# Kernel tuning notes

Measured on AMD Instinct MI355X. Metric: run time of the kernel, lower is better.

## Reference

```python
import jax, jax.numpy as jnp
import numpy as np

N, E, B, D, DEPTH = 20000, 160000, 16, 128, 5
L = 4 * DEPTH  # 20 EGNN layer calls: (ground, ground_to_sub, sub, sub_to_ground) x depth


def _ln(x, g, b):
    mu = jnp.mean(x, -1, keepdims=True)
    var = jnp.mean((x - mu) ** 2, -1, keepdims=True)
    return (x - mu) * jax.lax.rsqrt(var + 1e-5) * g + b


def setup_inputs() -> dict:
    key = jax.random.key(0)
    ks = jax.random.split(key, 24)

    def w(k, shape, fan_in):
        return jax.random.normal(k, shape, jnp.float32) / np.float32(np.sqrt(fan_in))

    return {
        "x": jax.random.normal(ks[0], (N, 1), jnp.float32),
        "pos": jax.random.normal(ks[1], (N, 3), jnp.float32),
        "edge_index": jax.random.randint(ks[2], (2, E), 0, N),
        "node_subnode_index": jax.random.randint(ks[3], (2, E), 0, N),
        "subgraph_edge_index": jax.random.randint(ks[4], (2, E), 0, N),
        "subnode_node_index": jax.random.randint(ks[5], (2, E), 0, N),
        "batch_ids": jnp.sort(jax.random.randint(ks[6], (N,), 0, B)),
        "emb_W": w(ks[7], (1, D), 1), "emb_b": jnp.zeros((D,), jnp.float32),
        # message MLP: Linear(2D+1,D) -> LN -> SiLU -> Linear(D,D) -> LN -> SiLU, stacked over L layers
        "Wm1": w(ks[8], (L, 2 * D + 1, D), 2 * D + 1), "bm1": jnp.zeros((L, D), jnp.float32),
        "gm1": jnp.ones((L, D), jnp.float32), "sm1": jnp.zeros((L, D), jnp.float32),
        "Wm2": w(ks[9], (L, D, D), D), "bm2": jnp.zeros((L, D), jnp.float32),
        "gm2": jnp.ones((L, D), jnp.float32), "sm2": jnp.zeros((L, D), jnp.float32),
        # update MLP: Linear(2D,D) -> LN -> SiLU -> Linear(D,D) -> LN -> SiLU
        "Wu1": w(ks[10], (L, 2 * D, D), 2 * D), "bu1": jnp.zeros((L, D), jnp.float32),
        "gu1": jnp.ones((L, D), jnp.float32), "su1": jnp.zeros((L, D), jnp.float32),
        "Wu2": w(ks[11], (L, D, D), D), "bu2": jnp.zeros((L, D), jnp.float32),
        "gu2": jnp.ones((L, D), jnp.float32), "su2": jnp.zeros((L, D), jnp.float32),
        # prediction head: Linear(D,D) -> ReLU -> Linear(D,1)
        "pred_W1": w(ks[12], (D, D), D), "pred_b1": jnp.zeros((D,), jnp.float32),
        "pred_W2": w(ks[13], (D, 1), D), "pred_b2": jnp.zeros((1,), jnp.float32),
    }


def _egnn(h, pos, ei, i, Wm1, bm1, gm1, sm1, Wm2, bm2, gm2, sm2,
          Wu1, bu1, gu1, su1, Wu2, bu2, gu2, su2):
    src, dst = ei[0], ei[1]          # PyG: messages flow source -> target
    rel = pos[dst] - pos[src]
    dist = jnp.sqrt(jnp.sum(rel * rel, -1, keepdims=True))  # [E,1]
    m = jnp.concatenate([h[dst], h[src], dist], -1)          # [E, 2D+1] = [h_i, h_j, d]
    m = jax.nn.silu(_ln(m @ Wm1[i] + bm1[i], gm1[i], sm1[i]))
    m = jax.nn.silu(_ln(m @ Wm2[i] + bm2[i], gm2[i], sm2[i]))
    agg = jax.ops.segment_sum(m, dst, num_segments=h.shape[0])
    u = jnp.concatenate([h, agg], -1)                        # [N, 2D]
    u = jax.nn.silu(_ln(u @ Wu1[i] + bu1[i], gu1[i], su1[i]))
    u = jax.nn.silu(_ln(u @ Wu2[i] + bu2[i], gu2[i], su2[i]))
    return u


def reference(x, pos, edge_index, node_subnode_index, subgraph_edge_index,
              subnode_node_index, batch_ids, emb_W, emb_b,
              Wm1, bm1, gm1, sm1, Wm2, bm2, gm2, sm2,
              Wu1, bu1, gu1, su1, Wu2, bu2, gu2, su2,
              pred_W1, pred_b1, pred_W2, pred_b2):
    p = (Wm1, bm1, gm1, sm1, Wm2, bm2, gm2, sm2,
         Wu1, bu1, gu1, su1, Wu2, bu2, gu2, su2)
    h = x @ emb_W + emb_b
    edge_sets = (edge_index, node_subnode_index, subgraph_edge_index, subnode_node_index)
    for layer_idx in range(DEPTH):
        h0 = h
        for r, ei in enumerate(edge_sets):
            h = _egnn(h, pos, ei, layer_idx * 4 + r, *p)
        h = h + h0  # residual across the 4 message-passing steps
    out = jax.ops.segment_sum(h, batch_ids, num_segments=B)  # global_add_pool
    return jax.nn.relu(out @ pred_W1 + pred_b1) @ pred_W2 + pred_b2
```

## Files before the change

### kernel.cpp

```cpp
#include <hip/hip_runtime.h>

#define NN 20000
#define NE 160000
#define NL 20

typedef float f32x4 __attribute__((ext_vector_type(4)));
typedef float f32x2 __attribute__((ext_vector_type(2)));
typedef __bf16 bf16x8 __attribute__((ext_vector_type(8)));
typedef __bf16 bf16x4 __attribute__((ext_vector_type(4)));

__device__ __forceinline__ float silu_f(float v) {
  return v * __builtin_amdgcn_rcpf(1.f + __expf(-v));
}

__global__ void pack_weights(const float* __restrict__ W, __bf16* __restrict__ out,
                             const int K, const int lstride, const int total) {
  const int idx = blockIdx.x * 256 + threadIdx.x;
  if (idx >= total) return;
  const int lane = idx & 63;
  const int nt = (idx >> 6) & 7;
  const int ktn = K >> 5;
  const int kt = (idx >> 9) % ktn;
  const int layer = (idx >> 9) / ktn;
  const int col = nt * 16 + (lane & 15);
  const int kb = kt * 32 + (lane >> 4) * 8;
  const float* src = W + (size_t)layer * lstride;
  __bf16* o = out + (size_t)idx * 8;
#pragma unroll
  for (int j = 0; j < 8; ++j) o[j] = (__bf16)src[(kb + j) * 128 + col];
}

__global__ void pack_w1pq(const float* __restrict__ Wm1, __bf16* __restrict__ out) {
  const int idx = blockIdx.x * 256 + threadIdx.x;
  const int lane = idx & 63;
  const int nt = (idx >> 6) & 15;
  const int kt = (idx >> 10) & 3;
  const int layer = idx >> 12;
  const int c = nt * 16 + (lane & 15);
  const int kb = kt * 32 + (lane >> 4) * 8;
  const float* src = Wm1 + (size_t)layer * 257 * 128;
  __bf16* o = out + (size_t)idx * 8;
#pragma unroll
  for (int j = 0; j < 8; ++j) {
    const int k = kb + j;
    o[j] = (__bf16)((c < 128) ? src[k * 128 + c] : src[(128 + k) * 128 + (c - 128)]);
  }
}

__global__ void embed_kernel(const float* __restrict__ x, const float* __restrict__ embW,
                             const float* __restrict__ embB,
                             float* __restrict__ h, float* __restrict__ h0,
                             __bf16* __restrict__ hbf) {
  const int idx = blockIdx.x * 256 + threadIdx.x;
  const int n = idx >> 7, d = idx & 127;
  const float v = x[n] * embW[d] + embB[d];
  h[idx] = v;
  h0[idx] = v;
  hbf[idx] = (__bf16)v;
}

__global__ void hist_kernel(const int* __restrict__ ei, int* __restrict__ deg) {
  const int e = blockIdx.x * 256 + threadIdx.x;
  atomicAdd(&deg[ei[NE + e]], 1);
}

__global__ void scan_kernel(const int* __restrict__ deg, int* __restrict__ rowstart) {
  __shared__ int part[1024];
  const int r = blockIdx.x, t = threadIdx.x;
  const int* d = deg + (size_t)r * NN;
  int* rs = rowstart + (size_t)r * NN;
  int loc[20];
  int cnt = 0;
#pragma unroll
  for (int j = 0; j < 20; ++j) {
    const int i = t * 20 + j;
    const int v = (i < NN) ? d[i] : 0;
    loc[j] = cnt; cnt += v;
  }
  part[t] = cnt;
  __syncthreads();
  for (int off = 1; off < 1024; off <<= 1) {
    const int v = (t >= off) ? part[t - off] : 0;
    __syncthreads();
    part[t] += v;
    __syncthreads();
  }
  const int excl = (t == 0) ? 0 : part[t - 1];
#pragma unroll
  for (int j = 0; j < 20; ++j) {
    const int i = t * 20 + j;
    if (i < NN) rs[i] = excl + loc[j];
  }
}

__global__ void fill_kernel(const int* __restrict__ ei, const int* __restrict__ rowstart,
                            int* __restrict__ cursor, int* __restrict__ eord) {
  const int e = blockIdx.x * 256 + threadIdx.x;
  const int d = ei[NE + e];
  const int p = atomicAdd(&cursor[d], 1);
  eord[rowstart[d] + p] = e;
}

__global__ __launch_bounds__(256) void pq_kernel(
    const __bf16* __restrict__ hbf, const __bf16* __restrict__ pqw,
    __bf16* __restrict__ pq) {
  __shared__ __bf16 T1s[4][2048];
  const int t = threadIdx.x, w = t >> 6, l = t & 63;
  const int lr = l & 15, lg = l >> 4;
  const int wid = blockIdx.x * 4 + w;
  const int n0 = (wid >> 1) * 16;
  const int half = wid & 1;
  char* T1 = (char*)T1s[w];

  const int node = n0 + lr;
  bf16x8 bq[4];
#pragma unroll
  for (int kt = 0; kt < 4; ++kt)
    bq[kt] = *(const bf16x8*)(hbf + (size_t)node * 128 + kt * 32 + lg * 8);

  f32x4 acc[8];
#pragma unroll
  for (int nt = 0; nt < 8; ++nt) acc[nt] = (f32x4)0.f;
#pragma unroll
  for (int kt = 0; kt < 4; ++kt) {
#pragma unroll
    for (int nt = 0; nt < 8; ++nt) {
      const bf16x8 a = *(const bf16x8*)(pqw + ((size_t)((kt * 16 + half * 8 + nt) * 64 + l)) * 8);
      acc[nt] = __builtin_amdgcn_mfma_f32_16x16x32_bf16(a, bq[kt], acc[nt], 0, 0, 0);
    }
  }
#pragma unroll
  for (int nt = 0; nt < 8; ++nt) {
    bf16x4 v;
#pragma unroll
    for (int r = 0; r < 4; ++r) v[r] = (__bf16)acc[nt][r];
    *(bf16x4*)(T1 + ((lr * 256 + nt * 32 + lg * 8) ^ ((lr & 7) << 4))) = v;
  }
  __builtin_amdgcn_s_waitcnt(0);
#pragma unroll
  for (int j = 0; j < 4; ++j) {
    const int row = j * 4 + lg;
    const uint4 v = *(const uint4*)(T1 + ((row * 256 + lr * 16) ^ ((row & 7) << 4)));
    *(uint4*)(pq + (size_t)(n0 + row) * 256 + half * 128 + lr * 8) = v;
  }
}

__global__ __launch_bounds__(1024, 4) void edge_msg_kernel(
    const __bf16* __restrict__ pq, const float* __restrict__ pos,
    const int* __restrict__ ei, __bf16* __restrict__ msg,
    const __bf16* __restrict__ w2p, const float* __restrict__ w1last,
    const float* __restrict__ bm1, const float* __restrict__ gm1, const float* __restrict__ sm1,
    const float* __restrict__ bm2, const float* __restrict__ gm2, const float* __restrict__ sm2) {
  extern __shared__ char lds[];
  {
    const int t = threadIdx.x;
    uint4* d = (uint4*)lds;
    const uint4* s2 = (const uint4*)w2p;
    d[t] = s2[t];
    d[t + 1024] = s2[t + 1024];
  }
  __syncthreads();

  const int t = threadIdx.x, w = t >> 6, l = t & 63;
  const int lr = l & 15, lg = l >> 4;
  char* W2L = lds;
  char* T1  = lds + 32768 + w * 4096;

  const int e0 = blockIdx.x * 256 + w * 16;
  const int es = ei[e0 + lr], ed = ei[NE + e0 + lr];
  const float dx = pos[ed * 3 + 0] - pos[es * 3 + 0];
  const float dy = pos[ed * 3 + 1] - pos[es * 3 + 1];
  const float dz = pos[ed * 3 + 2] - pos[es * 3 + 2];
  const float dist = sqrtf(dx * dx + dy * dy + dz * dz);

  float v[4][8];
#pragma unroll
  for (int kt = 0; kt < 4; ++kt) {
    const int d0 = kt * 32 + lg * 8;
    const bf16x8 pA = *(const bf16x8*)(pq + (size_t)ed * 256 + d0);
    const bf16x8 qA = *(const bf16x8*)(pq + (size_t)es * 256 + 128 + d0);
    const f32x4 wl0 = *(const f32x4*)(w1last + d0), wl1 = *(const f32x4*)(w1last + d0 + 4);
    const f32x4 bb0 = *(const f32x4*)(bm1 + d0),    bb1 = *(const f32x4*)(bm1 + d0 + 4);
#pragma unroll
    for (int j = 0; j < 4; ++j) {
      v[kt][j]     = (float)pA[j]     + (float)qA[j]     + dist * wl0[j] + bb0[j];
      v[kt][j + 4] = (float)pA[j + 4] + (float)qA[j + 4] + dist * wl1[j] + bb1[j];
    }
  }
  float s = 0.f, q = 0.f;
#pragma unroll
  for (int kt = 0; kt < 4; ++kt)
#pragma unroll
    for (int j = 0; j < 8; ++j) { const float x = v[kt][j]; s += x; q += x * x; }
  s += __shfl_xor(s, 16); q += __shfl_xor(q, 16);
  s += __shfl_xor(s, 32); q += __shfl_xor(q, 32);
  const float mu1 = s * 0.0078125f;
  const float rstd1 = rsqrtf(q * 0.0078125f - mu1 * mu1 + 1e-5f);
  bf16x8 bfrag[4];
#pragma unroll
  for (int kt = 0; kt < 4; ++kt) {
    const int d0 = kt * 32 + lg * 8;
    const f32x4 g0 = *(const f32x4*)(gm1 + d0), g1 = *(const f32x4*)(gm1 + d0 + 4);
    const f32x4 s0 = *(const f32x4*)(sm1 + d0), s1 = *(const f32x4*)(sm1 + d0 + 4);
    bf16x8 bf;
#pragma unroll
    for (int j = 0; j < 4; ++j) {
      bf[j]     = (__bf16)silu_f((v[kt][j]     - mu1) * rstd1 * g0[j] + s0[j]);
      bf[j + 4] = (__bf16)silu_f((v[kt][j + 4] - mu1) * rstd1 * g1[j] + s1[j]);
    }
    bfrag[kt] = bf;
  }
  f32x4 acc2[8];
#pragma unroll
  for (int nt = 0; nt < 8; ++nt)
    acc2[nt] = *(const f32x4*)(bm2 + nt * 16 + lg * 4);
#pragma unroll
  for (int kt = 0; kt < 4; ++kt) {
#pragma unroll
    for (int nt = 0; nt < 8; ++nt) {
      const bf16x8 a = *(const bf16x8*)(W2L + ((kt * 8 + nt) * 64 + l) * 16);
      acc2[nt] = __builtin_amdgcn_mfma_f32_16x16x32_bf16(a, bfrag[kt], acc2[nt], 0, 0, 0);
    }
  }
  float s2 = 0.f, q2 = 0.f;
#pragma unroll
  for (int nt = 0; nt < 8; ++nt)
#pragma unroll
    for (int r = 0; r < 4; ++r) { const float x = acc2[nt][r]; s2 += x; q2 += x * x; }
  s2 += __shfl_xor(s2, 16); q2 += __shfl_xor(q2, 16);
  s2 += __shfl_xor(s2, 32); q2 += __shfl_xor(q2, 32);
  const float mu2 = s2 * 0.0078125f;
  const float rstd2 = rsqrtf(q2 * 0.0078125f - mu2 * mu2 + 1e-5f);
#pragma unroll
  for (int nt = 0; nt < 8; ++nt) {
    const f32x4 g2 = *(const f32x4*)(gm2 + nt * 16 + lg * 4);
    const f32x4 b2 = *(const f32x4*)(sm2 + nt * 16 + lg * 4);
    bf16x4 pk;
#pragma unroll
    for (int r = 0; r < 4; ++r)
      pk[r] = (__bf16)silu_f((acc2[nt][r] - mu2) * rstd2 * g2[r] + b2[r]);
    *(bf16x4*)(T1 + ((lr * 256 + nt * 32 + lg * 8) ^ ((lr & 7) << 4))) = pk;
  }
  __builtin_amdgcn_s_waitcnt(0);
  char* mbase = (char*)(msg + (size_t)e0 * 128);
#pragma unroll
  for (int j = 0; j < 4; ++j) {
    const int row = j * 4 + lg;
    const uint4 val = *(const uint4*)(T1 + ((row * 256 + lr * 16) ^ ((row & 7) << 4)));
    *(uint4*)(mbase + j * 1024 + l * 16) = val;
  }
}

__global__ void gather_kernel(const __bf16* __restrict__ msg,
                              const int* __restrict__ rowstart, const int* __restrict__ deg,
                              const int* __restrict__ eord, float* __restrict__ agg) {
  const int t = blockIdx.x * 256 + threadIdx.x;
  const int n = t >> 6, pd = t & 63;
  const int s = rowstart[n], dg = deg[n];
  float a0 = 0.f, a1 = 0.f;
  int i = 0;
  for (; i + 2 <= dg; i += 2) {
    const unsigned v0 = *(const unsigned*)(msg + (size_t)eord[s + i] * 128 + pd * 2);
    const unsigned v1 = *(const unsigned*)(msg + (size_t)eord[s + i + 1] * 128 + pd * 2);
    a0 += __uint_as_float(v0 << 16) + __uint_as_float(v1 << 16);
    a1 += __uint_as_float(v0 & 0xFFFF0000u) + __uint_as_float(v1 & 0xFFFF0000u);
  }
  if (i < dg) {
    const unsigned v0 = *(const unsigned*)(msg + (size_t)eord[s + i] * 128 + pd * 2);
    a0 += __uint_as_float(v0 << 16);
    a1 += __uint_as_float(v0 & 0xFFFF0000u);
  }
  f32x2 o; o[0] = a0; o[1] = a1;
  *(f32x2*)(agg + (size_t)n * 128 + pd * 2) = o;
}

__global__ __launch_bounds__(256) void update_kernel(
    float* __restrict__ h, const float* __restrict__ aggv, __bf16* __restrict__ hbf,
    float* __restrict__ h0, const int mode,
    const __bf16* __restrict__ w1p, const __bf16* __restrict__ w2p,
    const float* __restrict__ bu1, const float* __restrict__ gu1, const float* __restrict__ su1,
    const float* __restrict__ bu2, const float* __restrict__ gu2, const float* __restrict__ su2) {
  __shared__ __bf16 T1s[4][16 * 128];
  const int t = threadIdx.x, w = t >> 6, l = t & 63;
  const int lr = l & 15, lg = l >> 4;
  char* T1 = (char*)T1s[w];
  const int n0 = blockIdx.x * 64 + w * 16;
  const int n = n0 + lr;
  const int valid = (n < NN);
  const int nc = valid ? n : 0;

  bf16x8 ah[4], af[4];
#pragma unroll
  for (int kt = 0; kt < 4; ++kt) {
    ah[kt] = *(const bf16x8*)(hbf + (size_t)nc * 128 + kt * 32 + lg * 8);
    const f32x4* pA = (const f32x4*)(aggv + (size_t)nc * 128 + kt * 32 + lg * 8);
    const f32x4 u0 = pA[0], u1 = pA[1];
#pragma unroll
    for (int j = 0; j < 4; ++j) {
      af[kt][j] = (__bf16)u0[j];
      af[kt][j + 4] = (__bf16)u1[j];
    }
  }
  f32x4 acc[8];
#pragma unroll
  for (int nt = 0; nt < 8; ++nt) {
    const float bb = bu1[nt * 16 + lr];
#pragma unroll
    for (int r = 0; r < 4; ++r) acc[nt][r] = bb;
  }
#pragma unroll
  for (int kt = 0; kt < 8; ++kt) {
    const bf16x8 a = (kt < 4) ? ah[kt] : af[kt - 4];
#pragma unroll
    for (int nt = 0; nt < 8; ++nt) {
      const bf16x8 b = *(const bf16x8*)(w1p + ((size_t)((kt * 8 + nt) * 64 + l)) * 8);
      acc[nt] = __builtin_amdgcn_mfma_f32_16x16x32_bf16(a, b, acc[nt], 0, 0, 0);
    }
  }
  {
    float g1c[8], s1c[8];
#pragma unroll
    for (int nt = 0; nt < 8; ++nt) { g1c[nt] = gu1[nt * 16 + lr]; s1c[nt] = su1[nt * 16 + lr]; }
#pragma unroll
    for (int r = 0; r < 4; ++r) {
      float s = 0.f, q = 0.f;
#pragma unroll
      for (int nt = 0; nt < 8; ++nt) { const float v = acc[nt][r]; s += v; q += v * v; }
#pragma unroll
      for (int m = 1; m < 16; m <<= 1) { s += __shfl_xor(s, m); q += __shfl_xor(q, m); }
      const float mu = s * 0.0078125f;
      const float rstd = rsqrtf(q * 0.0078125f - mu * mu + 1e-5f);
      const int row = lg * 4 + r;
#pragma unroll
      for (int nt = 0; nt < 8; ++nt) {
        float v = (acc[nt][r] - mu) * rstd * g1c[nt] + s1c[nt];
        v = silu_f(v);
        const int col = nt * 16 + lr;
        *(__bf16*)(T1 + ((row * 256 + col * 2) ^ ((row & 7) << 4))) = (__bf16)v;
      }
    }
  }
  __syncthreads();
  f32x4 acc2[8];
#pragma unroll
  for (int nt = 0; nt < 8; ++nt) {
    const float bb = bu2[nt * 16 + lr];
#pragma unroll
    for (int r = 0; r < 4; ++r) acc2[nt][r] = bb;
  }
#pragma unroll
  for (int kt = 0; kt < 4; ++kt) {
    const bf16x8 a = *(const bf16x8*)(T1 + ((lr * 256 + kt * 64 + lg * 16) ^ ((lr & 7) << 4)));
#pragma unroll
    for (int nt = 0; nt < 8; ++nt) {
      const bf16x8 b = *(const bf16x8*)(w2p + ((size_t)((kt * 8 + nt) * 64 + l)) * 8);
      acc2[nt] = __builtin_amdgcn_mfma_f32_16x16x32_bf16(a, b, acc2[nt], 0, 0, 0);
    }
  }
  {
    float g2c[8], s2c[8];
#pragma unroll
    for (int nt = 0; nt < 8; ++nt) { g2c[nt] = gu2[nt * 16 + lr]; s2c[nt] = su2[nt * 16 + lr]; }
#pragma unroll
    for (int r = 0; r < 4; ++r) {
      float s = 0.f, q = 0.f;
#pragma unroll
      for (int nt = 0; nt < 8; ++nt) { const float v = acc2[nt][r]; s += v; q += v * v; }
#pragma unroll
      for (int m = 1; m < 16; m <<= 1) { s += __shfl_xor(s, m); q += __shfl_xor(q, m); }
      const float mu = s * 0.0078125f;
      const float rstd = rsqrtf(q * 0.0078125f - mu * mu + 1e-5f);
      const int row = lg * 4 + r;
      const int nn = n0 + row;
      if (nn < NN) {
#pragma unroll
        for (int nt = 0; nt < 8; ++nt) {
          const int col = nt * 16 + lr;
          float v = (acc2[nt][r] - mu) * rstd * g2c[nt] + s2c[nt];
          v = silu_f(v);
          if (mode) v += h0[(size_t)nn * 128 + col];
          h[(size_t)nn * 128 + col] = v;
          hbf[(size_t)nn * 128 + col] = (__bf16)v;
          if (mode) h0[(size_t)nn * 128 + col] = v;
        }
      }
    }
  }
}

__global__ void pool_kernel(const float* __restrict__ h, const int* __restrict__ bid,
                            float* __restrict__ pooled) {
  const int d = threadIdx.x;
  const int n0 = blockIdx.x * 32;
  const int nend = (n0 + 32 < NN) ? (n0 + 32) : NN;
  float acc = 0.f;
  int cur = bid[n0];
  for (int n = n0; n < nend; ++n) {
    const int b = bid[n];
    if (b != cur) { atomicAdd(&pooled[cur * 128 + d], acc); acc = 0.f; cur = b; }
    acc += h[(size_t)n * 128 + d];
  }
  atomicAdd(&pooled[cur * 128 + d], acc);
}

__global__ void head_kernel(const float* __restrict__ pooled,
                            const float* __restrict__ W1, const float* __restrict__ b1,
                            const float* __restrict__ W2, const float* __restrict__ b2,
                            float* __restrict__ out) {
  __shared__ float buf[2];
  const int b = blockIdx.x, t = threadIdx.x;
  float s = b1[t];
  for (int k = 0; k < 128; ++k) s += pooled[b * 128 + k] * W1[k * 128 + t];
  s = fmaxf(s, 0.f) * W2[t];
#pragma unroll
  for (int m = 32; m >= 1; m >>= 1) s += __shfl_down(s, m);
  if ((t & 63) == 0) buf[t >> 6] = s;
  __syncthreads();
  if (t == 0) out[b] = buf[0] + buf[1] + b2[0];
}

extern "C" void kernel_launch(void* const* d_in, const int* in_sizes, int n_in,
                              void* d_out, int out_size, void* d_ws, size_t ws_size,
                              hipStream_t stream) {
  const float* x   = (const float*)d_in[0];
  const float* pos = (const float*)d_in[1];
  const int* eis[4] = {(const int*)d_in[2], (const int*)d_in[3],
                       (const int*)d_in[4], (const int*)d_in[5]};
  const int* bid = (const int*)d_in[6];
  const float* embW = (const float*)d_in[7];
  const float* embB = (const float*)d_in[8];
  const float* Wm1 = (const float*)d_in[9];
  const float* bm1 = (const float*)d_in[10];
  const float* gm1 = (const float*)d_in[11];
  const float* sm1 = (const float*)d_in[12];
  const float* Wm2 = (const float*)d_in[13];
  const float* bm2 = (const float*)d_in[14];
  const float* gm2 = (const float*)d_in[15];
  const float* sm2 = (const float*)d_in[16];
  const float* Wu1 = (const float*)d_in[17];
  const float* bu1 = (const float*)d_in[18];
  const float* gu1 = (const float*)d_in[19];
  const float* su1 = (const float*)d_in[20];
  const float* Wu2 = (const float*)d_in[21];
  const float* bu2 = (const float*)d_in[22];
  const float* gu2 = (const float*)d_in[23];
  const float* su2 = (const float*)d_in[24];
  const float* pW1 = (const float*)d_in[25];
  const float* pb1 = (const float*)d_in[26];
  const float* pW2 = (const float*)d_in[27];
  const float* pb2 = (const float*)d_in[28];
  float* out = (float*)d_out;

  char* wp = (char*)d_ws;
  float* h = (float*)wp;      wp += (size_t)NN * 128 * 4;
  float* h0 = (float*)wp;     wp += (size_t)NN * 128 * 4;
  float* agg = (float*)wp;    wp += (size_t)NN * 128 * 4;
  float* pooled = (float*)wp; wp += 16 * 128 * 4;
  __bf16* hbf = (__bf16*)wp;  wp += (size_t)NN * 128 * 2;
  __bf16* pq = (__bf16*)wp;   wp += (size_t)NN * 256 * 2;
  __bf16* msg = (__bf16*)wp;  wp += (size_t)NE * 128 * 2;
  __bf16* pqw = (__bf16*)wp;  wp += (size_t)NL * 32768 * 2;
  __bf16* w2p = (__bf16*)wp;  wp += (size_t)NL * 16384 * 2;
  __bf16* wu1p = (__bf16*)wp; wp += (size_t)NL * 32768 * 2;
  __bf16* wu2p = (__bf16*)wp; wp += (size_t)NL * 16384 * 2;
  int* deg = (int*)wp;        wp += (size_t)4 * NN * 4;
  int* cursor = (int*)wp;     wp += (size_t)4 * NN * 4;
  int* rowstart = (int*)wp;   wp += (size_t)4 * NN * 4;
  int* eord = (int*)wp;       wp += (size_t)4 * NE * 4;

  static int lds_attr_set = 0;
  if (!lds_attr_set) {
    hipFuncSetAttribute((const void*)edge_msg_kernel,
                        hipFuncAttributeMaxDynamicSharedMemorySize, 98304);
    lds_attr_set = 1;
  }

  pack_w1pq<<<320, 256, 0, stream>>>(Wm1, pqw);
  pack_weights<<<160, 256, 0, stream>>>(Wm2, w2p, 128, 128 * 128, NL * 4 * 8 * 64);
  pack_weights<<<320, 256, 0, stream>>>(Wu1, wu1p, 256, 256 * 128, NL * 8 * 8 * 64);
  pack_weights<<<160, 256, 0, stream>>>(Wu2, wu2p, 128, 128 * 128, NL * 4 * 8 * 64);

  hipMemsetAsync(deg, 0, (size_t)8 * NN * 4, stream);
  embed_kernel<<<(NN * 128) / 256, 256, 0, stream>>>(x, embW, embB, h, h0, hbf);
  for (int r = 0; r < 4; ++r)
    hist_kernel<<<NE / 256, 256, 0, stream>>>(eis[r], deg + (size_t)r * NN);
  scan_kernel<<<4, 1024, 0, stream>>>(deg, rowstart);
  for (int r = 0; r < 4; ++r)
    fill_kernel<<<NE / 256, 256, 0, stream>>>(eis[r], rowstart + (size_t)r * NN,
                                              cursor + (size_t)r * NN, eord + (size_t)r * NE);

  for (int layer = 0; layer < 5; ++layer) {
    for (int r = 0; r < 4; ++r) {
      const int i = layer * 4 + r;
      pq_kernel<<<625, 256, 0, stream>>>(hbf, pqw + (size_t)i * 32768, pq);
      edge_msg_kernel<<<NE / 256, 1024, 98304, stream>>>(
          pq, pos, eis[r], msg,
          w2p + (size_t)i * 16384,
          Wm1 + (size_t)i * 257 * 128 + 256 * 128,
          bm1 + i * 128, gm1 + i * 128, sm1 + i * 128,
          bm2 + i * 128, gm2 + i * 128, sm2 + i * 128);
      gather_kernel<<<(NN * 64) / 256, 256, 0, stream>>>(
          msg, rowstart + (size_t)r * NN, deg + (size_t)r * NN, eord + (size_t)r * NE, agg);
      update_kernel<<<(NN + 63) / 64, 256, 0, stream>>>(
          h, agg, hbf, h0, (r == 3) ? 1 : 0,
          wu1p + (size_t)i * 32768, wu2p + (size_t)i * 16384,
          bu1 + i * 128, gu1 + i * 128, su1 + i * 128,
          bu2 + i * 128, gu2 + i * 128, su2 + i * 128);
    }
  }

  hipMemsetAsync(pooled, 0, 16 * 128 * 4, stream);
  pool_kernel<<<(NN + 31) / 32, 128, 0, stream>>>(h, bid, pooled);
  head_kernel<<<16, 128, 0, stream>>>(pooled, pW1, pb1, pW2, pb2, out);
}
```

Baseline: 1.944 ms.

## Store aggregates in bf16, trim redundant h writes, and halve edge LDS staging

```diff
diff --git a/kernel.cpp b/kernel.cpp
--- a/kernel.cpp
+++ b/kernel.cpp
@@ -49,12 +49,10 @@
 
 __global__ void embed_kernel(const float* __restrict__ x, const float* __restrict__ embW,
                              const float* __restrict__ embB,
-                             float* __restrict__ h, float* __restrict__ h0,
-                             __bf16* __restrict__ hbf) {
+                             float* __restrict__ h0, __bf16* __restrict__ hbf) {
   const int idx = blockIdx.x * 256 + threadIdx.x;
   const int n = idx >> 7, d = idx & 127;
   const float v = x[n] * embW[d] + embB[d];
-  h[idx] = v;
   h0[idx] = v;
   hbf[idx] = (__bf16)v;
 }
@@ -136,7 +134,6 @@
     for (int r = 0; r < 4; ++r) v[r] = (__bf16)acc[nt][r];
     *(bf16x4*)(T1 + ((lr * 256 + nt * 32 + lg * 8) ^ ((lr & 7) << 4))) = v;
   }
-  __builtin_amdgcn_s_waitcnt(0);
 #pragma unroll
   for (int j = 0; j < 4; ++j) {
     const int row = j * 4 + lg;
@@ -164,7 +161,7 @@
   const int t = threadIdx.x, w = t >> 6, l = t & 63;
   const int lr = l & 15, lg = l >> 4;
   char* W2L = lds;
-  char* T1  = lds + 32768 + w * 4096;
+  char* T1  = lds + 32768 + w * 2048;
 
   const int e0 = blockIdx.x * 256 + w * 16;
   const int es = ei[e0 + lr], ed = ei[NE + e0 + lr];
@@ -232,28 +229,30 @@
   const float mu2 = s2 * 0.0078125f;
   const float rstd2 = rsqrtf(q2 * 0.0078125f - mu2 * mu2 + 1e-5f);
 #pragma unroll
-  for (int nt = 0; nt < 8; ++nt) {
-    const f32x4 g2 = *(const f32x4*)(gm2 + nt * 16 + lg * 4);
-    const f32x4 b2 = *(const f32x4*)(sm2 + nt * 16 + lg * 4);
-    bf16x4 pk;
-#pragma unroll
-    for (int r = 0; r < 4; ++r)
-      pk[r] = (__bf16)silu_f((acc2[nt][r] - mu2) * rstd2 * g2[r] + b2[r]);
-    *(bf16x4*)(T1 + ((lr * 256 + nt * 32 + lg * 8) ^ ((lr & 7) << 4))) = pk;
-  }
-  __builtin_amdgcn_s_waitcnt(0);
-  char* mbase = (char*)(msg + (size_t)e0 * 128);
-#pragma unroll
-  for (int j = 0; j < 4; ++j) {
-    const int row = j * 4 + lg;
-    const uint4 val = *(const uint4*)(T1 + ((row * 256 + lr * 16) ^ ((row & 7) << 4)));
-    *(uint4*)(mbase + j * 1024 + l * 16) = val;
+  for (int hh = 0; hh < 2; ++hh) {
+#pragma unroll
+    for (int nt4 = 0; nt4 < 4; ++nt4) {
+      const int nt = hh * 4 + nt4;
+      const f32x4 g2 = *(const f32x4*)(gm2 + nt * 16 + lg * 4);
+      const f32x4 b2 = *(const f32x4*)(sm2 + nt * 16 + lg * 4);
+      bf16x4 pk;
+#pragma unroll
+      for (int r = 0; r < 4; ++r)
+        pk[r] = (__bf16)silu_f((acc2[nt][r] - mu2) * rstd2 * g2[r] + b2[r]);
+      *(bf16x4*)(T1 + ((lr * 128 + nt4 * 32 + lg * 8) ^ ((lr & 7) << 4))) = pk;
+    }
+#pragma unroll
+    for (int j = 0; j < 2; ++j) {
+      const int e8 = j * 8 + (l >> 3);
+      const uint4 val = *(const uint4*)(T1 + ((e8 * 128 + (l & 7) * 16) ^ ((e8 & 7) << 4)));
+      *(uint4*)((char*)msg + (size_t)(e0 + e8) * 256 + hh * 128 + (l & 7) * 16) = val;
+    }
   }
 }
 
 __global__ void gather_kernel(const __bf16* __restrict__ msg,
                               const int* __restrict__ rowstart, const int* __restrict__ deg,
-                              const int* __restrict__ eord, float* __restrict__ agg) {
+                              const int* __restrict__ eord, __bf16* __restrict__ aggb) {
   const int t = blockIdx.x * 256 + threadIdx.x;
   const int n = t >> 6, pd = t & 63;
   const int s = rowstart[n], dg = deg[n];
@@ -270,12 +269,13 @@
     a0 += __uint_as_float(v0 << 16);
     a1 += __uint_as_float(v0 & 0xFFFF0000u);
   }
-  f32x2 o; o[0] = a0; o[1] = a1;
-  *(f32x2*)(agg + (size_t)n * 128 + pd * 2) = o;
+  __bf16 o0 = (__bf16)a0, o1 = (__bf16)a1;
+  unsigned pk = ((unsigned)*(unsigned short*)&o0) | (((unsigned)*(unsigned short*)&o1) << 16);
+  *(unsigned*)(aggb + (size_t)n * 128 + pd * 2) = pk;
 }
 
 __global__ __launch_bounds__(256) void update_kernel(
-    float* __restrict__ h, const float* __restrict__ aggv, __bf16* __restrict__ hbf,
+    float* __restrict__ h, const __bf16* __restrict__ aggb, __bf16* __restrict__ hbf,
     float* __restrict__ h0, const int mode,
     const __bf16* __restrict__ w1p, const __bf16* __restrict__ w2p,
     const float* __restrict__ bu1, const float* __restrict__ gu1, const float* __restrict__ su1,
@@ -293,13 +293,7 @@
 #pragma unroll
   for (int kt = 0; kt < 4; ++kt) {
     ah[kt] = *(const bf16x8*)(hbf + (size_t)nc * 128 + kt * 32 + lg * 8);
-    const f32x4* pA = (const f32x4*)(aggv + (size_t)nc * 128 + kt * 32 + lg * 8);
-    const f32x4 u0 = pA[0], u1 = pA[1];
-#pragma unroll
-    for (int j = 0; j < 4; ++j) {
-      af[kt][j] = (__bf16)u0[j];
-      af[kt][j + 4] = (__bf16)u1[j];
-    }
+    af[kt] = *(const bf16x8*)(aggb + (size_t)nc * 128 + kt * 32 + lg * 8);
   }
   f32x4 acc[8];
 #pragma unroll
@@ -340,7 +334,6 @@
       }
     }
   }
-  __syncthreads();
   f32x4 acc2[8];
 #pragma unroll
   for (int nt = 0; nt < 8; ++nt) {
@@ -378,10 +371,13 @@
           const int col = nt * 16 + lr;
           float v = (acc2[nt][r] - mu) * rstd * g2c[nt] + s2c[nt];
           v = silu_f(v);
-          if (mode) v += h0[(size_t)nn * 128 + col];
-          h[(size_t)nn * 128 + col] = v;
-          hbf[(size_t)nn * 128 + col] = (__bf16)v;
-          if (mode) h0[(size_t)nn * 128 + col] = v;
+          if (mode & 1) v += h0[(size_t)nn * 128 + col];
+          if (mode & 2) {
+            h[(size_t)nn * 128 + col] = v;
+          } else {
+            hbf[(size_t)nn * 128 + col] = (__bf16)v;
+            if (mode & 1) h0[(size_t)nn * 128 + col] = v;
+          }
         }
       }
     }
@@ -454,8 +450,8 @@
   char* wp = (char*)d_ws;
   float* h = (float*)wp;      wp += (size_t)NN * 128 * 4;
   float* h0 = (float*)wp;     wp += (size_t)NN * 128 * 4;
-  float* agg = (float*)wp;    wp += (size_t)NN * 128 * 4;
   float* pooled = (float*)wp; wp += 16 * 128 * 4;
+  __bf16* aggb = (__bf16*)wp; wp += (size_t)NN * 128 * 2;
   __bf16* hbf = (__bf16*)wp;  wp += (size_t)NN * 128 * 2;
   __bf16* pq = (__bf16*)wp;   wp += (size_t)NN * 256 * 2;
   __bf16* msg = (__bf16*)wp;  wp += (size_t)NE * 128 * 2;
@@ -471,7 +467,7 @@
   static int lds_attr_set = 0;
   if (!lds_attr_set) {
     hipFuncSetAttribute((const void*)edge_msg_kernel,
-                        hipFuncAttributeMaxDynamicSharedMemorySize, 98304);
+                        hipFuncAttributeMaxDynamicSharedMemorySize, 65536);
     lds_attr_set = 1;
   }
 
@@ -481,7 +477,7 @@
   pack_weights<<<160, 256, 0, stream>>>(Wu2, wu2p, 128, 128 * 128, NL * 4 * 8 * 64);
 
   hipMemsetAsync(deg, 0, (size_t)8 * NN * 4, stream);
-  embed_kernel<<<(NN * 128) / 256, 256, 0, stream>>>(x, embW, embB, h, h0, hbf);
+  embed_kernel<<<(NN * 128) / 256, 256, 0, stream>>>(x, embW, embB, h0, hbf);
   for (int r = 0; r < 4; ++r)
     hist_kernel<<<NE / 256, 256, 0, stream>>>(eis[r], deg + (size_t)r * NN);
   scan_kernel<<<4, 1024, 0, stream>>>(deg, rowstart);
@@ -492,17 +488,18 @@
   for (int layer = 0; layer < 5; ++layer) {
     for (int r = 0; r < 4; ++r) {
       const int i = layer * 4 + r;
+      const int mode = (r == 3) ? ((layer == 4) ? 3 : 1) : 0;
       pq_kernel<<<625, 256, 0, stream>>>(hbf, pqw + (size_t)i * 32768, pq);
-      edge_msg_kernel<<<NE / 256, 1024, 98304, stream>>>(
+      edge_msg_kernel<<<NE / 256, 1024, 65536, stream>>>(
           pq, pos, eis[r], msg,
           w2p + (size_t)i * 16384,
           Wm1 + (size_t)i * 257 * 128 + 256 * 128,
           bm1 + i * 128, gm1 + i * 128, sm1 + i * 128,
           bm2 + i * 128, gm2 + i * 128, sm2 + i * 128);
       gather_kernel<<<(NN * 64) / 256, 256, 0, stream>>>(
-          msg, rowstart + (size_t)r * NN, deg + (size_t)r * NN, eord + (size_t)r * NE, agg);
+          msg, rowstart + (size_t)r * NN, deg + (size_t)r * NN, eord + (size_t)r * NE, aggb);
       update_kernel<<<(NN + 63) / 64, 256, 0, stream>>>(
-          h, agg, hbf, h0, (r == 3) ? 1 : 0,
+          h, aggb, hbf, h0, mode,
           wu1p + (size_t)i * 32768, wu2p + (size_t)i * 16384,
           bu1 + i * 128, gu1 + i * 128, su1 + i * 128,
           bu2 + i * 128, gu2 + i * 128, su2 + i * 128);
```

Result: faster. 1.900 ms (-2.2%).
